# Kernel tuning notes

Hardware: AMD Instinct MI355X
Metric: run time of the kernel (lower is better)

Reference implementation:

```python
import jax, jax.numpy as jnp
import numpy as np

LN_EPS = 1e-5


def setup_inputs() -> dict:
    key = jax.random.key(0)
    ks = jax.random.split(key, 6)
    n_nodes, mem_dim = 500000, 256
    n_upd, msg_dim = 65536, 512
    return {
        "unique_node_ids": jnp.arange(n_upd, dtype=jnp.int64) if jax.config.jax_enable_x64 else jnp.arange(n_upd, dtype=jnp.int32),
        "unique_messages": jax.random.normal(ks[0], (n_upd, msg_dim), dtype=jnp.float32),
        "timestamps": jax.random.uniform(ks[1], (n_upd,), dtype=jnp.float32),
        "memory": jax.random.normal(ks[2], (n_nodes, mem_dim), dtype=jnp.float32),
        "last_update": jnp.zeros((n_nodes,), dtype=jnp.float32),
        "W_ih": jax.random.normal(ks[3], (3 * mem_dim, msg_dim), dtype=jnp.float32) * (1.0 / np.sqrt(msg_dim)),
        "W_hh": jax.random.normal(ks[4], (3 * mem_dim, mem_dim), dtype=jnp.float32) * (1.0 / np.sqrt(mem_dim)),
        "b_ih": jnp.zeros((3 * mem_dim,), dtype=jnp.float32),
        "b_hh": jnp.zeros((3 * mem_dim,), dtype=jnp.float32),
        "ln_gamma": jnp.ones((mem_dim,), dtype=jnp.float32),
        "ln_beta": jnp.zeros((mem_dim,), dtype=jnp.float32),
    }


def _gru_cell(x, h, W_ih, W_hh, b_ih, b_hh):
    # torch.nn.GRUCell math
    gi = x @ W_ih.T + b_ih          # [N, 3H]
    gh = h @ W_hh.T + b_hh          # [N, 3H]
    i_r, i_z, i_n = jnp.split(gi, 3, axis=-1)
    h_r, h_z, h_n = jnp.split(gh, 3, axis=-1)
    r = jax.nn.sigmoid(i_r + h_r)
    z = jax.nn.sigmoid(i_z + h_z)
    n = jnp.tanh(i_n + r * h_n)
    return (1.0 - z) * n + z * h


def _layer_norm(x, gamma, beta):
    mu = jnp.mean(x, axis=-1, keepdims=True)
    var = jnp.mean(jnp.square(x - mu), axis=-1, keepdims=True)
    return (x - mu) * jax.lax.rsqrt(var + LN_EPS) * gamma + beta


def reference(unique_node_ids, unique_messages, timestamps, memory, last_update,
              W_ih, W_hh, b_ih, b_hh, ln_gamma, ln_beta):
    # gather memory rows for the nodes being updated
    h = memory[unique_node_ids]                      # [N, H]
    new_h = _gru_cell(unique_messages, h, W_ih, W_hh, b_ih, b_hh)
    new_h = _layer_norm(new_h, ln_gamma, ln_beta)
    # scatter updated rows back (get_updated_memory semantics: pure copy)
    updated_memory = memory.at[unique_node_ids].set(new_h)
    updated_last_update = last_update.at[unique_node_ids].set(timestamps)
    return updated_memory, updated_last_update
```

## Files before the change

kernel.cpp:

```cpp
#include <hip/hip_runtime.h>
#include <hip/hip_bf16.h>

typedef float  f32x4 __attribute__((ext_vector_type(4)));
typedef short  s16x8 __attribute__((ext_vector_type(8)));

#define MEMH   256
#define MSGD   512
#define G3     768
#define W_IH_ELEMS (G3*MSGD)
#define W_HH_ELEMS (G3*MEMH)
#define W_TOT_ELEMS (W_IH_ELEMS + W_HH_ELEMS)
#define W_BYTES    ((size_t)W_TOT_ELEMS * 2)

#define BM     32
#define NTHR   512
#define AM_OFF 0
#define AH_OFF 32768
#define PART_OFF 49152
#define STAT_OFF 51200
#define LDS_BYTES 51456

static __device__ __forceinline__ short f2bf(float x) {
    __hip_bfloat16 b = __float2bfloat16(x);
    return __builtin_bit_cast(short, b);
}
static __device__ __forceinline__ float bf2f(short s) {
    unsigned int u = ((unsigned int)(unsigned short)s) << 16;
    return __builtin_bit_cast(float, u);
}
static __device__ __forceinline__ float sigf(float x) {
    return 1.f / (1.f + __expf(-x));
}
static __device__ __forceinline__ float tanh_fast(float x) {
    float e = __expf(-2.f * fabsf(x));
    float t = (1.f - e) / (1.f + e);
    return copysignf(t, x);
}
static __device__ __forceinline__ f32x4 ntload4(const float* p) {
    return __builtin_nontemporal_load((const f32x4*)p);
}
static __device__ __forceinline__ void ntstore4(float* p, f32x4 v) {
    __builtin_nontemporal_store(v, (f32x4*)p);
}

__global__ void smu_copy_kernel(const float* __restrict__ mem,
                                const float* __restrict__ lu,
                                float* __restrict__ out_mem,
                                float* __restrict__ out_lu,
                                long n_mem4, long n_lu4) {
    long i = (long)blockIdx.x * blockDim.x + threadIdx.x;
    long stride = (long)gridDim.x * blockDim.x;
    long total = n_mem4 + n_lu4;
    for (; i < total; i += stride) {
        if (i < n_mem4) ntstore4(out_mem + i * 4, ntload4(mem + i * 4));
        else {
            long j = (i - n_mem4) * 4;
            ntstore4(out_lu + j, ntload4(lu + j));
        }
    }
}

__global__ void smu_cvtw_kernel(const float* __restrict__ wih,
                                const float* __restrict__ whh,
                                short* __restrict__ o) {
    int i = blockIdx.x * blockDim.x + threadIdx.x;
    if (i >= W_TOT_ELEMS) return;
    if (i < W_IH_ELEMS) {
        int f = i >> 9, r = i & 511, l = r >> 3, e = r & 7;
        int t = f >> 4, k = f & 15;
        int row = t * 16 + (l & 15), col = k * 32 + (l >> 4) * 8 + e;
        o[i] = f2bf(wih[row * MSGD + col]);
    } else {
        int j = i - W_IH_ELEMS;
        int f = j >> 9, r = j & 511, l = r >> 3, e = r & 7;
        int t = f >> 3, k = f & 7;
        int row = t * 16 + (l & 15), col = k * 32 + (l >> 4) * 8 + e;
        o[i] = f2bf(whh[row * MEMH + col]);
    }
}

__global__ void smu_clear_kernel(unsigned* __restrict__ p, int n) {
    int i = blockIdx.x * blockDim.x + threadIdx.x;
    if (i < n) p[i] = 0u;
}
__global__ void smu_bits_kernel(const int* __restrict__ ids,
                                unsigned* __restrict__ bm, int n) {
    int i = blockIdx.x * blockDim.x + threadIdx.x;
    if (i < n) {
        int id = ids[i];
        atomicOr(&bm[id >> 5], 1u << (id & 31));
    }
}

template<bool USE_WS>
static __device__ __forceinline__ s16x8 load_b(const float* __restrict__ Wf,
                                               const short* __restrict__ Wb,
                                               int t, int k, int ldk, int nkt, int lane) {
    if constexpr (USE_WS) {
        return *(const s16x8*)(Wb + ((size_t)(t * nkt + k) << 9) + lane * 8);
    } else {
        int row = t * 16 + (lane & 15);
        int col = k * 32 + (lane >> 4) * 8;
        f32x4 x = *(const f32x4*)(Wf + (size_t)row * ldk + col);
        f32x4 y = *(const f32x4*)(Wf + (size_t)row * ldk + col + 4);
        s16x8 s;
        s[0]=f2bf(x[0]); s[1]=f2bf(x[1]); s[2]=f2bf(x[2]); s[3]=f2bf(x[3]);
        s[4]=f2bf(y[0]); s[5]=f2bf(y[1]); s[6]=f2bf(y[2]); s[7]=f2bf(y[3]);
        return s;
    }
}

template<bool USE_WS, bool SPLIT>
__global__ __launch_bounds__(NTHR, 4)
void smu_fused_kernel(const int*   __restrict__ ids,
                      const float* __restrict__ msg,
                      const float* __restrict__ ts,
                      const float* __restrict__ memory,
                      const float* __restrict__ lu,
                      const float* __restrict__ W_ih,
                      const float* __restrict__ W_hh,
                      const float* __restrict__ b_ih,
                      const float* __restrict__ b_hh,
                      const float* __restrict__ gamma,
                      const float* __restrict__ beta,
                      const short* __restrict__ wsw,
                      const unsigned* __restrict__ bm,
                      float* __restrict__ out_mem,
                      float* __restrict__ out_lu,
                      long n_nodes, int n_copy_blk) {
    __shared__ __align__(16) unsigned char lds[LDS_BYTES];
    const int tid = threadIdx.x;
    const int bid = blockIdx.x;

    int local;
    if constexpr (SPLIT) {
        const int s = bid >> 9;
        const int r = bid & 511;
        local = s * 256 + (r & 255);
        if (r >= 256) {
            const long nu     = n_nodes * (MEMH / 4);
            const long stride = (long)n_copy_blk * NTHR;
            const long i0     = (long)local * NTHR + tid;

            for (long i = i0; i < nu; i += stride * 4) {
                long  u0 = i, u1 = i + stride, u2 = i + stride * 2, u3 = i + stride * 3;
                f32x4 v0, v1, v2, v3;
                bool  f0 = false, f1 = false, f2 = false, f3 = false;
                {
                    long r0 = u0 >> 6;
                    f0 = !((bm[r0 >> 5] >> (r0 & 31)) & 1u);
                    if (f0) v0 = ntload4(memory + u0 * 4);
                }
                if (u1 < nu) {
                    long r1 = u1 >> 6;
                    f1 = !((bm[r1 >> 5] >> (r1 & 31)) & 1u);
                    if (f1) v1 = ntload4(memory + u1 * 4);
                }
                if (u2 < nu) {
                    long r2 = u2 >> 6;
                    f2 = !((bm[r2 >> 5] >> (r2 & 31)) & 1u);
                    if (f2) v2 = ntload4(memory + u2 * 4);
                }
                if (u3 < nu) {
                    long r3 = u3 >> 6;
                    f3 = !((bm[r3 >> 5] >> (r3 & 31)) & 1u);
                    if (f3) v3 = ntload4(memory + u3 * 4);
                }
                if (f0) ntstore4(out_mem + u0 * 4, v0);
                if (f1) ntstore4(out_mem + u1 * 4, v1);
                if (f2) ntstore4(out_mem + u2 * 4, v2);
                if (f3) ntstore4(out_mem + u3 * 4, v3);
            }
            for (long i = i0; i < n_nodes; i += stride) {
                if (!((bm[i >> 5] >> (i & 31)) & 1u)) {
                    float v = __builtin_nontemporal_load(lu + i);
                    __builtin_nontemporal_store(v, out_lu + i);
                }
            }
            return;
        }
    } else {
        local = bid;
    }

    const long base = (long)local * BM;

    {
        const float* src = msg + base * MSGD;
        #pragma unroll
        for (int it = 0; it < 4; ++it) {
            int u = tid + NTHR * it;
            int row = u >> 6;
            f32x4 a = ntload4(src + u * 8);
            f32x4 b = ntload4(src + u * 8 + 4);
            s16x8 s;
            s[0]=f2bf(a[0]); s[1]=f2bf(a[1]); s[2]=f2bf(a[2]); s[3]=f2bf(a[3]);
            s[4]=f2bf(b[0]); s[5]=f2bf(b[1]); s[6]=f2bf(b[2]); s[7]=f2bf(b[3]);
            int byte = AM_OFF + ((u * 16) ^ ((row & 7) << 4));
            *(s16x8*)(lds + byte) = s;
        }
        #pragma unroll
        for (int it = 0; it < 2; ++it) {
            int u = tid + NTHR * it;
            int row = u >> 5;
            int c8  = u & 31;
            int id  = ids[base + row];
            const float* hs = memory + (size_t)id * MEMH + c8 * 8;
            f32x4 a = ntload4(hs);
            f32x4 b = ntload4(hs + 4);
            s16x8 s;
            s[0]=f2bf(a[0]); s[1]=f2bf(a[1]); s[2]=f2bf(a[2]); s[3]=f2bf(a[3]);
            s[4]=f2bf(b[0]); s[5]=f2bf(b[1]); s[6]=f2bf(b[2]); s[7]=f2bf(b[3]);
            int byte = AH_OFF + ((u * 16) ^ ((row & 7) << 4));
            *(s16x8*)(lds + byte) = s;
        }
    }
    __syncthreads();

    const int lane = tid & 63;
    const int w    = tid >> 6;
    const int lr   = lane & 15;
    const int lk8  = (lane >> 4) * 8;
    const int sw   = (lr & 7) << 4;
    const short* Wi = wsw;
    const short* Wh = wsw + W_IH_ELEMS;

    f32x4 rz[2][2][2] = {};
    f32x4 gin[2][2]   = {};
    f32x4 ghn[2][2]   = {};

    {
        s16x8 b[2][6];
        #pragma unroll
        for (int i = 0; i < 6; ++i)
            b[0][i] = load_b<USE_WS>(W_ih, Wi, w + 8*(i/3) + 16*(i%3), 0, MSGD, 16, lane);
        #pragma unroll
        for (int i = 0; i < 6; ++i)
            b[1][i] = load_b<USE_WS>(W_ih, Wi, w + 8*(i/3) + 16*(i%3), 1, MSGD, 16, lane);
        #pragma unroll
        for (int k = 0; k < 16; ++k) {
            const int cb = (k * 32 + lk8) * 2;
            #pragma unroll
            for (int m = 0; m < 2; ++m) {
                s16x8 a = *(const s16x8*)(lds + AM_OFF + (((m*16 + lr) * 1024 + cb) ^ sw));
                #pragma unroll
                for (int ci = 0; ci < 2; ++ci) {
                    rz[m][ci][0] = __builtin_amdgcn_mfma_f32_16x16x32_bf16(a, b[k & 1][ci*3+0], rz[m][ci][0], 0, 0, 0);
                    rz[m][ci][1] = __builtin_amdgcn_mfma_f32_16x16x32_bf16(a, b[k & 1][ci*3+1], rz[m][ci][1], 0, 0, 0);
                    gin[m][ci]   = __builtin_amdgcn_mfma_f32_16x16x32_bf16(a, b[k & 1][ci*3+2], gin[m][ci],   0, 0, 0);
                }
            }
            if (k < 14) {
                #pragma unroll
                for (int i = 0; i < 6; ++i)
                    b[k & 1][i] = load_b<USE_WS>(W_ih, Wi, w + 8*(i/3) + 16*(i%3), k + 2, MSGD, 16, lane);
            }
        }
    }
    {
        s16x8 b[2][6];
        #pragma unroll
        for (int i = 0; i < 6; ++i)
            b[0][i] = load_b<USE_WS>(W_hh, Wh, w + 8*(i/3) + 16*(i%3), 0, MEMH, 8, lane);
        #pragma unroll
        for (int i = 0; i < 6; ++i)
            b[1][i] = load_b<USE_WS>(W_hh, Wh, w + 8*(i/3) + 16*(i%3), 1, MEMH, 8, lane);
        #pragma unroll
        for (int k = 0; k < 8; ++k) {
            const int cb = (k * 32 + lk8) * 2;
            #pragma unroll
            for (int m = 0; m < 2; ++m) {
                s16x8 a = *(const s16x8*)(lds + AH_OFF + (((m*16 + lr) * 512 + cb) ^ sw));
                #pragma unroll
                for (int ci = 0; ci < 2; ++ci) {
                    rz[m][ci][0] = __builtin_amdgcn_mfma_f32_16x16x32_bf16(a, b[k & 1][ci*3+0], rz[m][ci][0], 0, 0, 0);
                    rz[m][ci][1] = __builtin_amdgcn_mfma_f32_16x16x32_bf16(a, b[k & 1][ci*3+1], rz[m][ci][1], 0, 0, 0);
                    ghn[m][ci]   = __builtin_amdgcn_mfma_f32_16x16x32_bf16(a, b[k & 1][ci*3+2], ghn[m][ci],   0, 0, 0);
                }
            }
            if (k < 6) {
                #pragma unroll
                for (int i = 0; i < 6; ++i)
                    b[k & 1][i] = load_b<USE_WS>(W_hh, Wh, w + 8*(i/3) + 16*(i%3), k + 2, MEMH, 8, lane);
            }
        }
    }

    const int lq = (lane >> 4);
    f32x4 o_[2][2];
    {
        #pragma unroll
        for (int ci = 0; ci < 2; ++ci) {
            const int j = (w + 8*ci) * 16 + lr;
            const float br = b_ih[j]       + b_hh[j];
            const float bz = b_ih[256 + j] + b_hh[256 + j];
            const float bihn = b_ih[512 + j], bhhn = b_hh[512 + j];
            #pragma unroll
            for (int m = 0; m < 2; ++m) {
                #pragma unroll
                for (int q = 0; q < 4; ++q) {
                    int row = m * 16 + lq * 4 + q;
                    float r = sigf(rz[m][ci][0][q] + br);
                    float z = sigf(rz[m][ci][1][q] + bz);
                    float n = tanh_fast(gin[m][ci][q] + bihn + r * (ghn[m][ci][q] + bhhn));
                    float hv = bf2f(*(const short*)(lds + AH_OFF + ((row * 512 + j * 2) ^ ((row & 7) << 4))));
                    o_[m][ci][q] = (1.f - z) * n + z * hv;
                }
            }
        }
    }

    {
        float* part = (float*)(lds + PART_OFF);
        #pragma unroll
        for (int m = 0; m < 2; ++m) {
            #pragma unroll
            for (int q = 0; q < 4; ++q) {
                float v0 = o_[m][0][q], v1 = o_[m][1][q];
                float s1 = v0 + v1;
                float s2 = v0 * v0 + v1 * v1;
                #pragma unroll
                for (int mk = 1; mk < 16; mk <<= 1) {
                    s1 += __shfl_xor(s1, mk);
                    s2 += __shfl_xor(s2, mk);
                }
                if (lr == 0) {
                    int row = m * 16 + lq * 4 + q;
                    part[(row * 8 + w) * 2]     = s1;
                    part[(row * 8 + w) * 2 + 1] = s2;
                }
            }
        }
    }
    __syncthreads();

    if (w == 0 && lane < 32) {
        const float* part = (const float*)(lds + PART_OFF);
        float s1 = 0.f, s2 = 0.f;
        #pragma unroll
        for (int i = 0; i < 8; ++i) {
            s1 += part[(lane * 8 + i) * 2];
            s2 += part[(lane * 8 + i) * 2 + 1];
        }
        float mu  = s1 * (1.f / 256.f);
        float var = fmaxf(s2 * (1.f / 256.f) - mu * mu, 0.f);
        float inv = rsqrtf(var + 1e-5f);
        float* st = (float*)(lds + STAT_OFF);
        st[lane * 2]     = mu;
        st[lane * 2 + 1] = inv;
    }
    __syncthreads();

    {
        const float* st = (const float*)(lds + STAT_OFF);
        #pragma unroll
        for (int ci = 0; ci < 2; ++ci) {
            const int j = (w + 8*ci) * 16 + lr;
            const float ga = gamma[j], be = beta[j];
            #pragma unroll
            for (int m = 0; m < 2; ++m) {
                #pragma unroll
                for (int q = 0; q < 4; ++q) {
                    int row = m * 16 + lq * 4 + q;
                    float mu  = st[row * 2];
                    float inv = st[row * 2 + 1];
                    int id = ids[base + row];
                    float y = (o_[m][ci][q] - mu) * inv * ga + be;
                    __builtin_nontemporal_store(y, out_mem + (size_t)id * MEMH + j);
                }
            }
        }
        if (w == 0 && lane < 32) {
            int id = ids[base + lane];
            __builtin_nontemporal_store(ts[base + lane], out_lu + id);
        }
    }
}

extern "C" void kernel_launch(void* const* d_in, const int* in_sizes, int n_in,
                              void* d_out, int out_size, void* d_ws, size_t ws_size,
                              hipStream_t stream) {
    (void)n_in; (void)out_size;
    const int*   ids = (const int*)  d_in[0];
    const float* msg = (const float*)d_in[1];
    const float* ts  = (const float*)d_in[2];
    const float* mem = (const float*)d_in[3];
    const float* lu  = (const float*)d_in[4];
    const float* Wih = (const float*)d_in[5];
    const float* Whh = (const float*)d_in[6];
    const float* bih = (const float*)d_in[7];
    const float* bhh = (const float*)d_in[8];
    const float* gam = (const float*)d_in[9];
    const float* bet = (const float*)d_in[10];

    const int  n_upd   = in_sizes[0];
    const long n_nodes = (long)in_sizes[3] / MEMH;

    float* out_mem = (float*)d_out;
    float* out_lu  = out_mem + (size_t)n_nodes * MEMH;

    const int    bm_words     = (int)((n_nodes + 31) / 32) + 4;
    const size_t bm_bytes_pad = (size_t)bm_words * 4;
    const bool ws_w  = (d_ws != nullptr) && (ws_size >= W_BYTES);
    const bool ws_bm = (d_ws != nullptr) && (ws_size >= W_BYTES + bm_bytes_pad);

    short*    wsw = (short*)d_ws;
    unsigned* bm  = (unsigned*)((char*)d_ws + W_BYTES);

    const int grid_gru = n_upd / BM;

    if (ws_w) {
        smu_cvtw_kernel<<<(W_TOT_ELEMS + 255) / 256, 256, 0, stream>>>(Wih, Whh, wsw);
    }

    if (ws_bm) {
        smu_clear_kernel<<<(bm_words + 255) / 256, 256, 0, stream>>>(bm, bm_words);
        smu_bits_kernel<<<(n_upd + 255) / 256, 256, 0, stream>>>(ids, bm, n_upd);
        smu_fused_kernel<true, true><<<2 * grid_gru, NTHR, 0, stream>>>(
            ids, msg, ts, mem, lu, Wih, Whh, bih, bhh, gam, bet,
            wsw, bm, out_mem, out_lu, n_nodes, grid_gru);
    } else {
        long n_mem4 = n_nodes * (MEMH / 4);
        long n_lu4  = n_nodes / 4;
        smu_copy_kernel<<<2048, 256, 0, stream>>>(mem, lu, out_mem, out_lu, n_mem4, n_lu4);
        if (ws_w) {
            smu_fused_kernel<true, false><<<grid_gru, NTHR, 0, stream>>>(
                ids, msg, ts, mem, lu, Wih, Whh, bih, bhh, gam, bet,
                wsw, nullptr, out_mem, out_lu, n_nodes, 0);
        } else {
            smu_fused_kernel<false, false><<<grid_gru, NTHR, 0, stream>>>(
                ids, msg, ts, mem, lu, Wih, Whh, bih, bhh, gam, bet,
                nullptr, nullptr, out_mem, out_lu, n_nodes, 0);
        }
    }
}
```

Measured before the change: 344.8 us.

## Co-schedule copy and GRU warps in one 1024-thread block with LDS counter barrier

Each block now holds 1024 threads. The upper 512 threads do the bitmap-masked bulk memory copy with 8-way unrolled loads, and the lower 512 do the GRU tile. Before, copy and GRU ran as separate interleaved blocks. The second __syncthreads for the LayerNorm stats is replaced by an LDS atomic counter spin-wait among the 8 GRU waves, and each lane computes the row statistics itself. This is meant to overlap copy bandwidth with GRU compute inside each CU. The cost is lower occupancy (launch bounds 1), a spin-wait barrier, and a bigger per-thread unroll.

```diff
diff --git a/kernel.cpp b/kernel.cpp
--- a/kernel.cpp
+++ b/kernel.cpp
@@ -13,12 +13,12 @@
 #define W_BYTES    ((size_t)W_TOT_ELEMS * 2)
 
 #define BM     32
-#define NTHR   512
+#define NTHR   1024
 #define AM_OFF 0
 #define AH_OFF 32768
 #define PART_OFF 49152
-#define STAT_OFF 51200
-#define LDS_BYTES 51456
+#define CNT_OFF  51200
+#define LDS_BYTES 51264
 
 static __device__ __forceinline__ short f2bf(float x) {
     __hip_bfloat16 b = __float2bfloat16(x);
@@ -110,8 +110,8 @@
     }
 }
 
-template<bool USE_WS, bool SPLIT>
-__global__ __launch_bounds__(NTHR, 4)
+template<bool USE_WS, bool FUSED>
+__global__ __launch_bounds__(NTHR, 1)
 void smu_fused_kernel(const int*   __restrict__ ids,
                       const float* __restrict__ msg,
                       const float* __restrict__ ts,
@@ -127,68 +127,18 @@
                       const unsigned* __restrict__ bm,
                       float* __restrict__ out_mem,
                       float* __restrict__ out_lu,
-                      long n_nodes, int n_copy_blk) {
+                      long n_nodes) {
     __shared__ __align__(16) unsigned char lds[LDS_BYTES];
     const int tid = threadIdx.x;
     const int bid = blockIdx.x;
-
-    int local;
-    if constexpr (SPLIT) {
-        const int s = bid >> 9;
-        const int r = bid & 511;
-        local = s * 256 + (r & 255);
-        if (r >= 256) {
-            const long nu     = n_nodes * (MEMH / 4);
-            const long stride = (long)n_copy_blk * NTHR;
-            const long i0     = (long)local * NTHR + tid;
-
-            for (long i = i0; i < nu; i += stride * 4) {
-                long  u0 = i, u1 = i + stride, u2 = i + stride * 2, u3 = i + stride * 3;
-                f32x4 v0, v1, v2, v3;
-                bool  f0 = false, f1 = false, f2 = false, f3 = false;
-                {
-                    long r0 = u0 >> 6;
-                    f0 = !((bm[r0 >> 5] >> (r0 & 31)) & 1u);
-                    if (f0) v0 = ntload4(memory + u0 * 4);
-                }
-                if (u1 < nu) {
-                    long r1 = u1 >> 6;
-                    f1 = !((bm[r1 >> 5] >> (r1 & 31)) & 1u);
-                    if (f1) v1 = ntload4(memory + u1 * 4);
-                }
-                if (u2 < nu) {
-                    long r2 = u2 >> 6;
-                    f2 = !((bm[r2 >> 5] >> (r2 & 31)) & 1u);
-                    if (f2) v2 = ntload4(memory + u2 * 4);
-                }
-                if (u3 < nu) {
-                    long r3 = u3 >> 6;
-                    f3 = !((bm[r3 >> 5] >> (r3 & 31)) & 1u);
-                    if (f3) v3 = ntload4(memory + u3 * 4);
-                }
-                if (f0) ntstore4(out_mem + u0 * 4, v0);
-                if (f1) ntstore4(out_mem + u1 * 4, v1);
-                if (f2) ntstore4(out_mem + u2 * 4, v2);
-                if (f3) ntstore4(out_mem + u3 * 4, v3);
-            }
-            for (long i = i0; i < n_nodes; i += stride) {
-                if (!((bm[i >> 5] >> (i & 31)) & 1u)) {
-                    float v = __builtin_nontemporal_load(lu + i);
-                    __builtin_nontemporal_store(v, out_lu + i);
-                }
-            }
-            return;
-        }
-    } else {
-        local = bid;
-    }
-
-    const long base = (long)local * BM;
+    const long base = (long)bid * BM;
+
+    if (tid == 0) *(unsigned*)(lds + CNT_OFF) = 0u;
 
     {
         const float* src = msg + base * MSGD;
         #pragma unroll
-        for (int it = 0; it < 4; ++it) {
+        for (int it = 0; it < 2; ++it) {
             int u = tid + NTHR * it;
             int row = u >> 6;
             f32x4 a = ntload4(src + u * 8);
@@ -199,9 +149,8 @@
             int byte = AM_OFF + ((u * 16) ^ ((row & 7) << 4));
             *(s16x8*)(lds + byte) = s;
         }
-        #pragma unroll
-        for (int it = 0; it < 2; ++it) {
-            int u = tid + NTHR * it;
+        {
+            int u = tid;
             int row = u >> 5;
             int c8  = u & 31;
             int id  = ids[base + row];
@@ -217,6 +166,41 @@
     }
     __syncthreads();
 
+    if (tid >= 512) {
+        if constexpr (FUSED) {
+            const long nu     = n_nodes * (MEMH / 4);
+            const long stride = (long)gridDim.x * 512;
+            const long i0     = (long)bid * 512 + (tid - 512);
+
+            for (long i = i0; i < nu; i += stride * 8) {
+                f32x4 v[8];
+                bool  f[8];
+                #pragma unroll
+                for (int j = 0; j < 8; ++j) {
+                    long u = i + stride * j;
+                    f[j] = false;
+                    if (u < nu) {
+                        long r = u >> 6;
+                        f[j] = !((bm[r >> 5] >> (r & 31)) & 1u);
+                        if (f[j]) v[j] = ntload4(memory + u * 4);
+                    }
+                }
+                #pragma unroll
+                for (int j = 0; j < 8; ++j) {
+                    long u = i + stride * j;
+                    if (f[j]) ntstore4(out_mem + u * 4, v[j]);
+                }
+            }
+            for (long i = i0; i < n_nodes; i += stride) {
+                if (!((bm[i >> 5] >> (i & 31)) & 1u)) {
+                    float v = __builtin_nontemporal_load(lu + i);
+                    __builtin_nontemporal_store(v, out_lu + i);
+                }
+            }
+        }
+        return;
+    }
+
     const int lane = tid & 63;
     const int w    = tid >> 6;
     const int lr   = lane & 15;
@@ -332,27 +316,38 @@
             }
         }
     }
-    __syncthreads();
-
-    if (w == 0 && lane < 32) {
+
+    __threadfence_block();
+    if (lane == 0) atomicAdd((unsigned*)(lds + CNT_OFF), 1u);
+    {
+        volatile unsigned* cp = (volatile unsigned*)(lds + CNT_OFF);
+        while (*cp < 8u) __builtin_amdgcn_s_sleep(2);
+    }
+    __threadfence_block();
+
+    float mu_[2][4], inv_[2][4];
+    {
         const float* part = (const float*)(lds + PART_OFF);
-        float s1 = 0.f, s2 = 0.f;
-        #pragma unroll
-        for (int i = 0; i < 8; ++i) {
-            s1 += part[(lane * 8 + i) * 2];
-            s2 += part[(lane * 8 + i) * 2 + 1];
-        }
-        float mu  = s1 * (1.f / 256.f);
-        float var = fmaxf(s2 * (1.f / 256.f) - mu * mu, 0.f);
-        float inv = rsqrtf(var + 1e-5f);
-        float* st = (float*)(lds + STAT_OFF);
-        st[lane * 2]     = mu;
-        st[lane * 2 + 1] = inv;
-    }
-    __syncthreads();
-
-    {
-        const float* st = (const float*)(lds + STAT_OFF);
+        #pragma unroll
+        for (int m = 0; m < 2; ++m) {
+            #pragma unroll
+            for (int q = 0; q < 4; ++q) {
+                int row = m * 16 + lq * 4 + q;
+                float s1 = 0.f, s2 = 0.f;
+                #pragma unroll
+                for (int i = 0; i < 8; ++i) {
+                    s1 += part[(row * 8 + i) * 2];
+                    s2 += part[(row * 8 + i) * 2 + 1];
+                }
+                float mu  = s1 * (1.f / 256.f);
+                float var = fmaxf(s2 * (1.f / 256.f) - mu * mu, 0.f);
+                mu_[m][q]  = mu;
+                inv_[m][q] = rsqrtf(var + 1e-5f);
+            }
+        }
+    }
+
+    {
         #pragma unroll
         for (int ci = 0; ci < 2; ++ci) {
             const int j = (w + 8*ci) * 16 + lr;
@@ -362,10 +357,8 @@
                 #pragma unroll
                 for (int q = 0; q < 4; ++q) {
                     int row = m * 16 + lq * 4 + q;
-                    float mu  = st[row * 2];
-                    float inv = st[row * 2 + 1];
                     int id = ids[base + row];
-                    float y = (o_[m][ci][q] - mu) * inv * ga + be;
+                    float y = (o_[m][ci][q] - mu_[m][q]) * inv_[m][q] * ga + be;
                     __builtin_nontemporal_store(y, out_mem + (size_t)id * MEMH + j);
                 }
             }
@@ -407,7 +400,7 @@
     short*    wsw = (short*)d_ws;
     unsigned* bm  = (unsigned*)((char*)d_ws + W_BYTES);
 
-    const int grid_gru = n_upd / BM;
+    const int grid = n_upd / BM;
 
     if (ws_w) {
         smu_cvtw_kernel<<<(W_TOT_ELEMS + 255) / 256, 256, 0, stream>>>(Wih, Whh, wsw);
@@ -416,21 +409,21 @@
     if (ws_bm) {
         smu_clear_kernel<<<(bm_words + 255) / 256, 256, 0, stream>>>(bm, bm_words);
         smu_bits_kernel<<<(n_upd + 255) / 256, 256, 0, stream>>>(ids, bm, n_upd);
-        smu_fused_kernel<true, true><<<2 * grid_gru, NTHR, 0, stream>>>(
+        smu_fused_kernel<true, true><<<grid, NTHR, 0, stream>>>(
             ids, msg, ts, mem, lu, Wih, Whh, bih, bhh, gam, bet,
-            wsw, bm, out_mem, out_lu, n_nodes, grid_gru);
+            wsw, bm, out_mem, out_lu, n_nodes);
     } else {
         long n_mem4 = n_nodes * (MEMH / 4);
         long n_lu4  = n_nodes / 4;
         smu_copy_kernel<<<2048, 256, 0, stream>>>(mem, lu, out_mem, out_lu, n_mem4, n_lu4);
         if (ws_w) {
-            smu_fused_kernel<true, false><<<grid_gru, NTHR, 0, stream>>>(
+            smu_fused_kernel<true, false><<<grid, NTHR, 0, stream>>>(
                 ids, msg, ts, mem, lu, Wih, Whh, bih, bhh, gam, bet,
-                wsw, nullptr, out_mem, out_lu, n_nodes, 0);
+                wsw, nullptr, out_mem, out_lu, n_nodes);
         } else {
-            smu_fused_kernel<false, false><<<grid_gru, NTHR, 0, stream>>>(
+            smu_fused_kernel<false, false><<<grid, NTHR, 0, stream>>>(
                 ids, msg, ts, mem, lu, Wih, Whh, bih, bhh, gam, bet,
-                nullptr, nullptr, out_mem, out_lu, n_nodes, 0);
-        }
-    }
-}
+                nullptr, nullptr, out_mem, out_lu, n_nodes);
+        }
+    }
+}
```

After: 377.9 us. 9.6% more time.

## Double GRU row tile to 64 with 16 waves and interleave copy blocks

Applied to the files above, without the earlier changes.

Grows the GRU block from 32 rows and 512 threads to 64 rows and 1024 threads. Each of the 16 waves now owns one 16-column slice for all 64 rows, so every loaded weight fragment feeds twice as many MFMAs and global weight traffic per update row is halved. Copy and GRU blocks now alternate by block-index parity instead of the fixed 256/256 split, and the LayerNorm reduction becomes a per-wave shuffle reduction. The cost is about 107KB of LDS per block and launch bounds of 1, which lowers occupancy and limits latency hiding for the copy blocks.

```diff
diff --git a/kernel.cpp b/kernel.cpp
--- a/kernel.cpp
+++ b/kernel.cpp
@@ -12,13 +12,13 @@
 #define W_TOT_ELEMS (W_IH_ELEMS + W_HH_ELEMS)
 #define W_BYTES    ((size_t)W_TOT_ELEMS * 2)
 
-#define BM     32
-#define NTHR   512
+#define BM     64
+#define NTHR   1024
 #define AM_OFF 0
-#define AH_OFF 32768
-#define PART_OFF 49152
-#define STAT_OFF 51200
-#define LDS_BYTES 51456
+#define AH_OFF 65536
+#define PART_OFF 98304
+#define STAT_OFF 106496
+#define LDS_BYTES 107008
 
 static __device__ __forceinline__ short f2bf(float x) {
     __hip_bfloat16 b = __float2bfloat16(x);
@@ -27,6 +27,12 @@
 static __device__ __forceinline__ float bf2f(short s) {
     unsigned int u = ((unsigned int)(unsigned short)s) << 16;
     return __builtin_bit_cast(float, u);
+}
+static __device__ __forceinline__ s16x8 cvt8(f32x4 a, f32x4 b) {
+    s16x8 s;
+    s[0]=f2bf(a[0]); s[1]=f2bf(a[1]); s[2]=f2bf(a[2]); s[3]=f2bf(a[3]);
+    s[4]=f2bf(b[0]); s[5]=f2bf(b[1]); s[6]=f2bf(b[2]); s[7]=f2bf(b[3]);
+    return s;
 }
 static __device__ __forceinline__ float sigf(float x) {
     return 1.f / (1.f + __expf(-x));
@@ -103,15 +109,12 @@
         int col = k * 32 + (lane >> 4) * 8;
         f32x4 x = *(const f32x4*)(Wf + (size_t)row * ldk + col);
         f32x4 y = *(const f32x4*)(Wf + (size_t)row * ldk + col + 4);
-        s16x8 s;
-        s[0]=f2bf(x[0]); s[1]=f2bf(x[1]); s[2]=f2bf(x[2]); s[3]=f2bf(x[3]);
-        s[4]=f2bf(y[0]); s[5]=f2bf(y[1]); s[6]=f2bf(y[2]); s[7]=f2bf(y[3]);
-        return s;
-    }
-}
-
-template<bool USE_WS, bool SPLIT>
-__global__ __launch_bounds__(NTHR, 4)
+        return cvt8(x, y);
+    }
+}
+
+template<bool USE_WS, bool FUSED>
+__global__ __launch_bounds__(NTHR, 1)
 void smu_fused_kernel(const int*   __restrict__ ids,
                       const float* __restrict__ msg,
                       const float* __restrict__ ts,
@@ -127,63 +130,57 @@
                       const unsigned* __restrict__ bm,
                       float* __restrict__ out_mem,
                       float* __restrict__ out_lu,
-                      long n_nodes, int n_copy_blk) {
+                      long n_nodes) {
     __shared__ __align__(16) unsigned char lds[LDS_BYTES];
     const int tid = threadIdx.x;
     const int bid = blockIdx.x;
 
-    int local;
-    if constexpr (SPLIT) {
-        const int s = bid >> 9;
-        const int r = bid & 511;
-        local = s * 256 + (r & 255);
-        if (r >= 256) {
-            const long nu     = n_nodes * (MEMH / 4);
-            const long stride = (long)n_copy_blk * NTHR;
-            const long i0     = (long)local * NTHR + tid;
-
-            for (long i = i0; i < nu; i += stride * 4) {
-                long  u0 = i, u1 = i + stride, u2 = i + stride * 2, u3 = i + stride * 3;
-                f32x4 v0, v1, v2, v3;
-                bool  f0 = false, f1 = false, f2 = false, f3 = false;
-                {
-                    long r0 = u0 >> 6;
-                    f0 = !((bm[r0 >> 5] >> (r0 & 31)) & 1u);
-                    if (f0) v0 = ntload4(memory + u0 * 4);
-                }
-                if (u1 < nu) {
-                    long r1 = u1 >> 6;
-                    f1 = !((bm[r1 >> 5] >> (r1 & 31)) & 1u);
-                    if (f1) v1 = ntload4(memory + u1 * 4);
-                }
-                if (u2 < nu) {
-                    long r2 = u2 >> 6;
-                    f2 = !((bm[r2 >> 5] >> (r2 & 31)) & 1u);
-                    if (f2) v2 = ntload4(memory + u2 * 4);
-                }
-                if (u3 < nu) {
-                    long r3 = u3 >> 6;
-                    f3 = !((bm[r3 >> 5] >> (r3 & 31)) & 1u);
-                    if (f3) v3 = ntload4(memory + u3 * 4);
-                }
-                if (f0) ntstore4(out_mem + u0 * 4, v0);
-                if (f1) ntstore4(out_mem + u1 * 4, v1);
-                if (f2) ntstore4(out_mem + u2 * 4, v2);
-                if (f3) ntstore4(out_mem + u3 * 4, v3);
-            }
-            for (long i = i0; i < n_nodes; i += stride) {
-                if (!((bm[i >> 5] >> (i & 31)) & 1u)) {
-                    float v = __builtin_nontemporal_load(lu + i);
-                    __builtin_nontemporal_store(v, out_lu + i);
-                }
-            }
-            return;
-        }
-    } else {
-        local = bid;
-    }
-
-    const long base = (long)local * BM;
+    if (FUSED && (bid & 1)) {
+        const long nblk   = gridDim.x >> 1;
+        const long cid    = bid >> 1;
+        const long nu     = n_nodes * (MEMH / 4);
+        const long stride = nblk * NTHR;
+        const long i0     = cid * NTHR + tid;
+
+        for (long i = i0; i < nu; i += stride * 4) {
+            long  u0 = i, u1 = i + stride, u2 = i + stride * 2, u3 = i + stride * 3;
+            f32x4 v0, v1, v2, v3;
+            bool  f0 = false, f1 = false, f2 = false, f3 = false;
+            {
+                long r0 = u0 >> 6;
+                f0 = !((bm[r0 >> 5] >> (r0 & 31)) & 1u);
+                if (f0) v0 = ntload4(memory + u0 * 4);
+            }
+            if (u1 < nu) {
+                long r1 = u1 >> 6;
+                f1 = !((bm[r1 >> 5] >> (r1 & 31)) & 1u);
+                if (f1) v1 = ntload4(memory + u1 * 4);
+            }
+            if (u2 < nu) {
+                long r2 = u2 >> 6;
+                f2 = !((bm[r2 >> 5] >> (r2 & 31)) & 1u);
+                if (f2) v2 = ntload4(memory + u2 * 4);
+            }
+            if (u3 < nu) {
+                long r3 = u3 >> 6;
+                f3 = !((bm[r3 >> 5] >> (r3 & 31)) & 1u);
+                if (f3) v3 = ntload4(memory + u3 * 4);
+            }
+            if (f0) ntstore4(out_mem + u0 * 4, v0);
+            if (f1) ntstore4(out_mem + u1 * 4, v1);
+            if (f2) ntstore4(out_mem + u2 * 4, v2);
+            if (f3) ntstore4(out_mem + u3 * 4, v3);
+        }
+        for (long i = i0; i < n_nodes; i += stride) {
+            if (!((bm[i >> 5] >> (i & 31)) & 1u)) {
+                float v = __builtin_nontemporal_load(lu + i);
+                __builtin_nontemporal_store(v, out_lu + i);
+            }
+        }
+        return;
+    }
+
+    const long base = (long)(FUSED ? (bid >> 1) : bid) * BM;
 
     {
         const float* src = msg + base * MSGD;
@@ -193,11 +190,8 @@
             int row = u >> 6;
             f32x4 a = ntload4(src + u * 8);
             f32x4 b = ntload4(src + u * 8 + 4);
-            s16x8 s;
-            s[0]=f2bf(a[0]); s[1]=f2bf(a[1]); s[2]=f2bf(a[2]); s[3]=f2bf(a[3]);
-            s[4]=f2bf(b[0]); s[5]=f2bf(b[1]); s[6]=f2bf(b[2]); s[7]=f2bf(b[3]);
             int byte = AM_OFF + ((u * 16) ^ ((row & 7) << 4));
-            *(s16x8*)(lds + byte) = s;
+            *(s16x8*)(lds + byte) = cvt8(a, b);
         }
         #pragma unroll
         for (int it = 0; it < 2; ++it) {
@@ -208,11 +202,8 @@
             const float* hs = memory + (size_t)id * MEMH + c8 * 8;
             f32x4 a = ntload4(hs);
             f32x4 b = ntload4(hs + 4);
-            s16x8 s;
-            s[0]=f2bf(a[0]); s[1]=f2bf(a[1]); s[2]=f2bf(a[2]); s[3]=f2bf(a[3]);
-            s[4]=f2bf(b[0]); s[5]=f2bf(b[1]); s[6]=f2bf(b[2]); s[7]=f2bf(b[3]);
             int byte = AH_OFF + ((u * 16) ^ ((row & 7) << 4));
-            *(s16x8*)(lds + byte) = s;
+            *(s16x8*)(lds + byte) = cvt8(a, b);
         }
     }
     __syncthreads();
@@ -220,105 +211,90 @@
     const int lane = tid & 63;
     const int w    = tid >> 6;
     const int lr   = lane & 15;
-    const int lk8  = (lane >> 4) * 8;
+    const int lq   = lane >> 4;
+    const int lk8  = lq * 8;
     const int sw   = (lr & 7) << 4;
     const short* Wi = wsw;
     const short* Wh = wsw + W_IH_ELEMS;
 
-    f32x4 rz[2][2][2] = {};
-    f32x4 gin[2][2]   = {};
-    f32x4 ghn[2][2]   = {};
-
-    {
-        s16x8 b[2][6];
-        #pragma unroll
-        for (int i = 0; i < 6; ++i)
-            b[0][i] = load_b<USE_WS>(W_ih, Wi, w + 8*(i/3) + 16*(i%3), 0, MSGD, 16, lane);
-        #pragma unroll
-        for (int i = 0; i < 6; ++i)
-            b[1][i] = load_b<USE_WS>(W_ih, Wi, w + 8*(i/3) + 16*(i%3), 1, MSGD, 16, lane);
+    f32x4 acc[4][3] = {};
+    f32x4 accn[4]   = {};
+
+    {
+        s16x8 b[2][3];
+        #pragma unroll
+        for (int i = 0; i < 3; ++i) b[0][i] = load_b<USE_WS>(W_ih, Wi, w + 16*i, 0, MSGD, 16, lane);
+        #pragma unroll
+        for (int i = 0; i < 3; ++i) b[1][i] = load_b<USE_WS>(W_ih, Wi, w + 16*i, 1, MSGD, 16, lane);
         #pragma unroll
         for (int k = 0; k < 16; ++k) {
             const int cb = (k * 32 + lk8) * 2;
             #pragma unroll
-            for (int m = 0; m < 2; ++m) {
+            for (int m = 0; m < 4; ++m) {
                 s16x8 a = *(const s16x8*)(lds + AM_OFF + (((m*16 + lr) * 1024 + cb) ^ sw));
                 #pragma unroll
-                for (int ci = 0; ci < 2; ++ci) {
-                    rz[m][ci][0] = __builtin_amdgcn_mfma_f32_16x16x32_bf16(a, b[k & 1][ci*3+0], rz[m][ci][0], 0, 0, 0);
-                    rz[m][ci][1] = __builtin_amdgcn_mfma_f32_16x16x32_bf16(a, b[k & 1][ci*3+1], rz[m][ci][1], 0, 0, 0);
-                    gin[m][ci]   = __builtin_amdgcn_mfma_f32_16x16x32_bf16(a, b[k & 1][ci*3+2], gin[m][ci],   0, 0, 0);
-                }
+                for (int i = 0; i < 3; ++i)
+                    acc[m][i] = __builtin_amdgcn_mfma_f32_16x16x32_bf16(a, b[k & 1][i], acc[m][i], 0, 0, 0);
             }
             if (k < 14) {
                 #pragma unroll
-                for (int i = 0; i < 6; ++i)
-                    b[k & 1][i] = load_b<USE_WS>(W_ih, Wi, w + 8*(i/3) + 16*(i%3), k + 2, MSGD, 16, lane);
-            }
-        }
-    }
-    {
-        s16x8 b[2][6];
-        #pragma unroll
-        for (int i = 0; i < 6; ++i)
-            b[0][i] = load_b<USE_WS>(W_hh, Wh, w + 8*(i/3) + 16*(i%3), 0, MEMH, 8, lane);
-        #pragma unroll
-        for (int i = 0; i < 6; ++i)
-            b[1][i] = load_b<USE_WS>(W_hh, Wh, w + 8*(i/3) + 16*(i%3), 1, MEMH, 8, lane);
+                for (int i = 0; i < 3; ++i)
+                    b[k & 1][i] = load_b<USE_WS>(W_ih, Wi, w + 16*i, k + 2, MSGD, 16, lane);
+            }
+        }
+    }
+    {
+        s16x8 b[2][3];
+        #pragma unroll
+        for (int i = 0; i < 3; ++i) b[0][i] = load_b<USE_WS>(W_hh, Wh, w + 16*i, 0, MEMH, 8, lane);
+        #pragma unroll
+        for (int i = 0; i < 3; ++i) b[1][i] = load_b<USE_WS>(W_hh, Wh, w + 16*i, 1, MEMH, 8, lane);
         #pragma unroll
         for (int k = 0; k < 8; ++k) {
             const int cb = (k * 32 + lk8) * 2;
             #pragma unroll
-            for (int m = 0; m < 2; ++m) {
+            for (int m = 0; m < 4; ++m) {
                 s16x8 a = *(const s16x8*)(lds + AH_OFF + (((m*16 + lr) * 512 + cb) ^ sw));
-                #pragma unroll
-                for (int ci = 0; ci < 2; ++ci) {
-                    rz[m][ci][0] = __builtin_amdgcn_mfma_f32_16x16x32_bf16(a, b[k & 1][ci*3+0], rz[m][ci][0], 0, 0, 0);
-                    rz[m][ci][1] = __builtin_amdgcn_mfma_f32_16x16x32_bf16(a, b[k & 1][ci*3+1], rz[m][ci][1], 0, 0, 0);
-                    ghn[m][ci]   = __builtin_amdgcn_mfma_f32_16x16x32_bf16(a, b[k & 1][ci*3+2], ghn[m][ci],   0, 0, 0);
-                }
+                acc[m][0] = __builtin_amdgcn_mfma_f32_16x16x32_bf16(a, b[k & 1][0], acc[m][0], 0, 0, 0);
+                acc[m][1] = __builtin_amdgcn_mfma_f32_16x16x32_bf16(a, b[k & 1][1], acc[m][1], 0, 0, 0);
+                accn[m]   = __builtin_amdgcn_mfma_f32_16x16x32_bf16(a, b[k & 1][2], accn[m],   0, 0, 0);
             }
             if (k < 6) {
                 #pragma unroll
-                for (int i = 0; i < 6; ++i)
-                    b[k & 1][i] = load_b<USE_WS>(W_hh, Wh, w + 8*(i/3) + 16*(i%3), k + 2, MEMH, 8, lane);
-            }
-        }
-    }
-
-    const int lq = (lane >> 4);
-    f32x4 o_[2][2];
-    {
-        #pragma unroll
-        for (int ci = 0; ci < 2; ++ci) {
-            const int j = (w + 8*ci) * 16 + lr;
-            const float br = b_ih[j]       + b_hh[j];
-            const float bz = b_ih[256 + j] + b_hh[256 + j];
-            const float bihn = b_ih[512 + j], bhhn = b_hh[512 + j];
-            #pragma unroll
-            for (int m = 0; m < 2; ++m) {
-                #pragma unroll
-                for (int q = 0; q < 4; ++q) {
-                    int row = m * 16 + lq * 4 + q;
-                    float r = sigf(rz[m][ci][0][q] + br);
-                    float z = sigf(rz[m][ci][1][q] + bz);
-                    float n = tanh_fast(gin[m][ci][q] + bihn + r * (ghn[m][ci][q] + bhhn));
-                    float hv = bf2f(*(const short*)(lds + AH_OFF + ((row * 512 + j * 2) ^ ((row & 7) << 4))));
-                    o_[m][ci][q] = (1.f - z) * n + z * hv;
-                }
-            }
-        }
-    }
-
-    {
-        float* part = (float*)(lds + PART_OFF);
-        #pragma unroll
-        for (int m = 0; m < 2; ++m) {
+                for (int i = 0; i < 3; ++i)
+                    b[k & 1][i] = load_b<USE_WS>(W_hh, Wh, w + 16*i, k + 2, MEMH, 8, lane);
+            }
+        }
+    }
+
+    const int j = w * 16 + lr;
+    f32x4 o_[4];
+    {
+        const float br = b_ih[j]       + b_hh[j];
+        const float bz = b_ih[256 + j] + b_hh[256 + j];
+        const float bihn = b_ih[512 + j], bhhn = b_hh[512 + j];
+        #pragma unroll
+        for (int m = 0; m < 4; ++m) {
             #pragma unroll
             for (int q = 0; q < 4; ++q) {
-                float v0 = o_[m][0][q], v1 = o_[m][1][q];
-                float s1 = v0 + v1;
-                float s2 = v0 * v0 + v1 * v1;
+                int row = m * 16 + lq * 4 + q;
+                float r = sigf(acc[m][0][q] + br);
+                float z = sigf(acc[m][1][q] + bz);
+                float n = tanh_fast(acc[m][2][q] + bihn + r * (accn[m][q] + bhhn));
+                float hv = bf2f(*(const short*)(lds + AH_OFF + ((row * 512 + j * 2) ^ ((row & 7) << 4))));
+                o_[m][q] = (1.f - z) * n + z * hv;
+            }
+        }
+    }
+
+    {
+        float* part = (float*)(lds + PART_OFF);
+        #pragma unroll
+        for (int m = 0; m < 4; ++m) {
+            #pragma unroll
+            for (int q = 0; q < 4; ++q) {
+                float v = o_[m][q];
+                float s1 = v, s2 = v * v;
                 #pragma unroll
                 for (int mk = 1; mk < 16; mk <<= 1) {
                     s1 += __shfl_xor(s1, mk);
@@ -326,51 +302,50 @@
                 }
                 if (lr == 0) {
                     int row = m * 16 + lq * 4 + q;
-                    part[(row * 8 + w) * 2]     = s1;
-                    part[(row * 8 + w) * 2 + 1] = s2;
+                    part[(row * 16 + w) * 2]     = s1;
+                    part[(row * 16 + w) * 2 + 1] = s2;
                 }
             }
         }
     }
     __syncthreads();
 
-    if (w == 0 && lane < 32) {
+    {
         const float* part = (const float*)(lds + PART_OFF);
-        float s1 = 0.f, s2 = 0.f;
-        #pragma unroll
-        for (int i = 0; i < 8; ++i) {
-            s1 += part[(lane * 8 + i) * 2];
-            s2 += part[(lane * 8 + i) * 2 + 1];
-        }
-        float mu  = s1 * (1.f / 256.f);
-        float var = fmaxf(s2 * (1.f / 256.f) - mu * mu, 0.f);
-        float inv = rsqrtf(var + 1e-5f);
-        float* st = (float*)(lds + STAT_OFF);
-        st[lane * 2]     = mu;
-        st[lane * 2 + 1] = inv;
+        int row = w * 4 + lq;
+        float s1 = part[(row * 16 + lr) * 2];
+        float s2 = part[(row * 16 + lr) * 2 + 1];
+        #pragma unroll
+        for (int mk = 1; mk < 16; mk <<= 1) {
+            s1 += __shfl_xor(s1, mk);
+            s2 += __shfl_xor(s2, mk);
+        }
+        if (lr == 0) {
+            float mu  = s1 * (1.f / 256.f);
+            float var = fmaxf(s2 * (1.f / 256.f) - mu * mu, 0.f);
+            float* st = (float*)(lds + STAT_OFF);
+            st[row * 2]     = mu;
+            st[row * 2 + 1] = rsqrtf(var + 1e-5f);
+        }
     }
     __syncthreads();
 
     {
         const float* st = (const float*)(lds + STAT_OFF);
-        #pragma unroll
-        for (int ci = 0; ci < 2; ++ci) {
-            const int j = (w + 8*ci) * 16 + lr;
-            const float ga = gamma[j], be = beta[j];
+        const float ga = gamma[j], be = beta[j];
+        #pragma unroll
+        for (int m = 0; m < 4; ++m) {
             #pragma unroll
-            for (int m = 0; m < 2; ++m) {
-                #pragma unroll
-                for (int q = 0; q < 4; ++q) {
-                    int row = m * 16 + lq * 4 + q;
-                    float mu  = st[row * 2];
-                    float inv = st[row * 2 + 1];
-                    int id = ids[base + row];
-                    float y = (o_[m][ci][q] - mu) * inv * ga + be;
-                    __builtin_nontemporal_store(y, out_mem + (size_t)id * MEMH + j);
-                }
-            }
-        }
-        if (w == 0 && lane < 32) {
+            for (int q = 0; q < 4; ++q) {
+                int row = m * 16 + lq * 4 + q;
+                float mu  = st[row * 2];
+                float inv = st[row * 2 + 1];
+                int id = ids[base + row];
+                float y = (o_[m][q] - mu) * inv * ga + be;
+                __builtin_nontemporal_store(y, out_mem + (size_t)id * MEMH + j);
+            }
+        }
+        if (w == 0) {
             int id = ids[base + lane];
             __builtin_nontemporal_store(ts[base + lane], out_lu + id);
         }
@@ -407,7 +382,7 @@
     short*    wsw = (short*)d_ws;
     unsigned* bm  = (unsigned*)((char*)d_ws + W_BYTES);
 
-    const int grid_gru = n_upd / BM;
+    const int grid = n_upd / BM;
 
     if (ws_w) {
         smu_cvtw_kernel<<<(W_TOT_ELEMS + 255) / 256, 256, 0, stream>>>(Wih, Whh, wsw);
@@ -416,21 +391,21 @@
     if (ws_bm) {
         smu_clear_kernel<<<(bm_words + 255) / 256, 256, 0, stream>>>(bm, bm_words);
         smu_bits_kernel<<<(n_upd + 255) / 256, 256, 0, stream>>>(ids, bm, n_upd);
-        smu_fused_kernel<true, true><<<2 * grid_gru, NTHR, 0, stream>>>(
+        smu_fused_kernel<true, true><<<2 * grid, NTHR, 0, stream>>>(
             ids, msg, ts, mem, lu, Wih, Whh, bih, bhh, gam, bet,
-            wsw, bm, out_mem, out_lu, n_nodes, grid_gru);
+            wsw, bm, out_mem, out_lu, n_nodes);
     } else {
         long n_mem4 = n_nodes * (MEMH / 4);
         long n_lu4  = n_nodes / 4;
         smu_copy_kernel<<<2048, 256, 0, stream>>>(mem, lu, out_mem, out_lu, n_mem4, n_lu4);
         if (ws_w) {
-            smu_fused_kernel<true, false><<<grid_gru, NTHR, 0, stream>>>(
+            smu_fused_kernel<true, false><<<grid, NTHR, 0, stream>>>(
                 ids, msg, ts, mem, lu, Wih, Whh, bih, bhh, gam, bet,
-                wsw, nullptr, out_mem, out_lu, n_nodes, 0);
+                wsw, nullptr, out_mem, out_lu, n_nodes);
         } else {
-            smu_fused_kernel<false, false><<<grid_gru, NTHR, 0, stream>>>(
+            smu_fused_kernel<false, false><<<grid, NTHR, 0, stream>>>(
                 ids, msg, ts, mem, lu, Wih, Whh, bih, bhh, gam, bet,
-                nullptr, nullptr, out_mem, out_lu, n_nodes, 0);
-        }
-    }
-}
+                nullptr, nullptr, out_mem, out_lu, n_nodes);
+        }
+    }
+}
```

Measured after the change: 339.0 us. No clear change (-1.7%).
